# Kernel optimization log

Hardware: AMD Instinct MI355X
Metric: run time of the kernel (lower is better)

## Reference

```python
import jax, jax.numpy as jnp
import numpy as np

L, H, E, V, BS = 12, 12, 768, 50257, 1024  # layers, heads, n_embd, vocab, block_size
B, T = 2, 1024
D = E // H


def setup_inputs() -> dict:
    key = jax.random.key(0)
    ks = jax.random.split(key, 10)
    s = 0.02
    d = {}
    d["idx"] = jax.random.randint(ks[0], (B, T), 0, V)
    d["targets"] = jax.random.randint(ks[1], (B, T), 0, V)
    # embeddings (wte tied with lm_head)
    d["wte"] = (jax.random.normal(ks[2], (V, E)) * s).astype(jnp.float32)
    d["wpe"] = (jax.random.normal(ks[3], (BS, E)) * s).astype(jnp.float32)
    # stacked per-layer params; Linear weights stored [in, out] (= torch W.T)
    d["ln1_w"] = jnp.ones((L, E), jnp.float32)
    d["ln1_b"] = jnp.zeros((L, E), jnp.float32)
    d["attn_w"] = (jax.random.normal(ks[4], (L, E, 3 * E)) * s).astype(jnp.float32)
    d["attn_b"] = jnp.zeros((L, 3 * E), jnp.float32)
    d["proj_w"] = (jax.random.normal(ks[5], (L, E, E)) * s).astype(jnp.float32)
    d["proj_b"] = jnp.zeros((L, E), jnp.float32)
    d["ln2_w"] = jnp.ones((L, E), jnp.float32)
    d["ln2_b"] = jnp.zeros((L, E), jnp.float32)
    d["fc_w"] = (jax.random.normal(ks[6], (L, E, 4 * E)) * s).astype(jnp.float32)
    d["fc_b"] = jnp.zeros((L, 4 * E), jnp.float32)
    d["fcproj_w"] = (jax.random.normal(ks[7], (L, 4 * E, E)) * s).astype(jnp.float32)
    d["fcproj_b"] = jnp.zeros((L, E), jnp.float32)
    d["lnf_w"] = jnp.ones((E,), jnp.float32)
    d["lnf_b"] = jnp.zeros((E,), jnp.float32)
    return d


def _ln(x, w, b, eps=1e-5):
    m = jnp.mean(x, -1, keepdims=True)
    v = jnp.mean(jnp.square(x - m), -1, keepdims=True)
    return (x - m) * jax.lax.rsqrt(v + eps) * w + b


def _block(x, p, mask):
    l1w, l1b, aw, ab, pw, pb, l2w, l2b, fw, fb, fpw, fpb = p
    Bx, Tx, C = x.shape
    # causal self-attention (explicit QK^T + mask + softmax + AV, as in source)
    qkv = _ln(x, l1w, l1b) @ aw + ab                       # [B,T,3E]
    q, k, v = jnp.split(qkv, 3, axis=-1)
    q = q.reshape(Bx, Tx, H, D).transpose(0, 2, 1, 3)       # [B,H,T,D]
    k = k.reshape(Bx, Tx, H, D).transpose(0, 2, 1, 3)
    v = v.reshape(Bx, Tx, H, D).transpose(0, 2, 1, 3)
    att = jnp.einsum('bhqd,bhkd->bhqk', q, k) * (1.0 / np.sqrt(D))
    att = jnp.where(mask, att, -jnp.inf)
    att = jax.nn.softmax(att, axis=-1)
    y = jnp.einsum('bhqk,bhkd->bhqd', att, v)
    y = y.transpose(0, 2, 1, 3).reshape(Bx, Tx, C)
    x = x + y @ pw + pb
    # MLP with tanh-approx GELU
    h = jax.nn.gelu(_ln(x, l2w, l2b) @ fw + fb, approximate=True)
    x = x + h @ fpw + fpb
    return x


def reference(idx, targets, wte, wpe, ln1_w, ln1_b, attn_w, attn_b, proj_w, proj_b,
              ln2_w, ln2_b, fc_w, fc_b, fcproj_w, fcproj_b, lnf_w, lnf_b):
    Tq = idx.shape[1]
    x = wte[idx] + wpe[:Tq]                                 # [B,T,E]
    mask = jnp.tril(jnp.ones((Tq, Tq), dtype=bool))

    def step(x, p):
        return _block(x, p, mask), None

    layer_params = (ln1_w, ln1_b, attn_w, attn_b, proj_w, proj_b,
                    ln2_w, ln2_b, fc_w, fc_b, fcproj_w, fcproj_b)
    x, _ = jax.lax.scan(step, x, layer_params)
    x = _ln(x, lnf_w, lnf_b)
    logits = x @ wte.T                                      # tied lm_head, [B,T,V]
    logp = jax.nn.log_softmax(logits, axis=-1)
    nll = -jnp.take_along_axis(logp, targets[..., None], axis=-1)[..., 0]
    loss = jnp.mean(nll)
    return logits, loss
```

## Files before the change

### kernel.cpp

```cpp
#include <hip/hip_runtime.h>
#include <hip/hip_bf16.h>
#include <math.h>

#define LNUM 12
#define HNUM 12
#define EDIM 768
#define VDIM 50257
#define BDIM 2
#define TDIM 1024
#define BT (BDIM*TDIM)
#define E3 (3*EDIM)
#define E4 (4*EDIM)
#define NPB (2*((VDIM+127)/128))

typedef __bf16 bf16x8 __attribute__((ext_vector_type(8)));
typedef float f32x4 __attribute__((ext_vector_type(4)));

__device__ __forceinline__ float gelu_f(float x) {
    float u = 0.7978845608028654f * (x + 0.044715f * x * x * x);
    return 0.5f * x * (1.0f + tanhf(u));
}

__device__ __forceinline__ void gl16(const void* g, void* l) {
    __builtin_amdgcn_global_load_lds(
        (const __attribute__((address_space(1))) unsigned int*)g,
        (__attribute__((address_space(3))) unsigned int*)l,
        16, 0, 0);
}

__global__ __launch_bounds__(256) void embed_kernel(
    const int* __restrict__ idx, const float* __restrict__ wte,
    const float* __restrict__ wpe, float* __restrict__ x)
{
    const int row = blockIdx.x;
    const int t = row % TDIM;
    const int tok = idx[row];
    const float* we = wte + (size_t)tok * EDIM;
    const float* pe = wpe + (size_t)t * EDIM;
    float* xr = x + (size_t)row * EDIM;
    for (int e = threadIdx.x; e < EDIM; e += 256) xr[e] = we[e] + pe[e];
}

__global__ __launch_bounds__(256) void ln_kernel(
    const float* __restrict__ in, const float* __restrict__ w,
    const float* __restrict__ b, __bf16* __restrict__ out)
{
    const int row = blockIdx.x, tid = threadIdx.x;
    const float* xr = in + (size_t)row * EDIM;
    float v0 = xr[tid], v1 = xr[tid + 256], v2 = xr[tid + 512];
    float s = v0 + v1 + v2;
    __shared__ float red[8];
    const int lane = tid & 63, wid = tid >> 6;
    #pragma unroll
    for (int off = 32; off; off >>= 1) s += __shfl_xor(s, off);
    if (lane == 0) red[wid] = s;
    __syncthreads();
    const float mean = (red[0] + red[1] + red[2] + red[3]) * (1.0f / EDIM);
    float d0 = v0 - mean, d1 = v1 - mean, d2 = v2 - mean;
    float s2 = d0 * d0 + d1 * d1 + d2 * d2;
    #pragma unroll
    for (int off = 32; off; off >>= 1) s2 += __shfl_xor(s2, off);
    if (lane == 0) red[4 + wid] = s2;
    __syncthreads();
    const float var = (red[4] + red[5] + red[6] + red[7]) * (1.0f / EDIM);
    const float inv = rsqrtf(var + 1e-5f);
    __bf16* orow = out + (size_t)row * EDIM;
    orow[tid]       = (__bf16)(d0 * inv * w[tid]       + b[tid]);
    orow[tid + 256] = (__bf16)(d1 * inv * w[tid + 256] + b[tid + 256]);
    orow[tid + 512] = (__bf16)(d2 * inv * w[tid + 512] + b[tid + 512]);
}

__global__ __launch_bounds__(256) void convt_kernel(
    const float* __restrict__ in, __bf16* __restrict__ out, int K, int N)
{
    in  += (size_t)blockIdx.z * K * N;
    out += (size_t)blockIdx.z * K * N;
    __shared__ float t[32][33];
    const int n0 = blockIdx.x * 32, k0 = blockIdx.y * 32;
    const int tx = threadIdx.x & 31, ty = threadIdx.x >> 5;
    #pragma unroll
    for (int r = ty; r < 32; r += 8)
        t[r][tx] = in[(size_t)(k0 + r) * N + n0 + tx];
    __syncthreads();
    #pragma unroll
    for (int r = ty; r < 32; r += 8)
        out[(size_t)(n0 + r) * K + k0 + tx] = (__bf16)t[tx][r];
}

__global__ __launch_bounds__(256) void cvt_kernel(
    const float* __restrict__ in, __bf16* __restrict__ out, long n4)
{
    for (long i = blockIdx.x * 256L + threadIdx.x; i < n4; i += (long)gridDim.x * 256L) {
        float4 v = ((const float4*)in)[i];
        out[i * 4 + 0] = (__bf16)v.x;
        out[i * 4 + 1] = (__bf16)v.y;
        out[i * 4 + 2] = (__bf16)v.z;
        out[i * 4 + 3] = (__bf16)v.w;
    }
}

template<int BM, int BN, int BK, bool BIAS, bool GELU_, bool RES_, bool OUTBF, bool NGUARD, bool LOGITS>
__global__ __launch_bounds__(256) void mgemm(
    const __bf16* __restrict__ A, const __bf16* __restrict__ Bt,
    const float* __restrict__ bias, const float* __restrict__ res,
    void* __restrict__ Cout, float* __restrict__ part, int M, int N, int K)
{
    constexpr int WM = BM / 2, WN = BN / 2;
    constexpr int FM = WM / 16, FN = WN / 16;
    constexpr int KS = BK / 32;
    constexpr int TB = BM * BK * 2;
    constexpr int rA = TB / 4096, rB = (BN * BK * 2) / 4096;
    constexpr int RPI = 2048 / BK;
    constexpr int CPR = BK / 8;
    __shared__ __align__(16) __bf16 As[3 * BM * BK];
    __shared__ __align__(16) __bf16 Bs[3 * BN * BK];
    const int tid = threadIdx.x;
    const int lane = tid & 63;
    const int wave = tid >> 6;
    const int wr = wave >> 1, wc = wave & 1;

    int bm, bn;
    if (LOGITS) {
        const int wg = blockIdx.x;
        bn = (wg & 7) + ((wg >> 7) << 3);
        bm = (wg >> 3) & 15;
        if (bn * BN >= N) return;
    } else { bm = blockIdx.y; bn = blockIdx.x; }
    const int m0 = bm * BM;
    const int n0 = bn * BN;

    const int srow = tid / CPR;
    const int skey = (BK == 32) ? ((srow >> 1) & 3) : (srow & 7);
    const int c0 = (tid % CPR) ^ skey;

    const __bf16* gA = A + (size_t)(m0 + srow) * K + c0 * 8;
    const __bf16* gB[rB];
    #pragma unroll
    for (int r = 0; r < rB; ++r) {
        int nr = n0 + srow + r * RPI;
        if (NGUARD) nr = nr < N ? nr : N - 1;
        gB[r] = Bt + (size_t)nr * K + c0 * 8;
    }

    const int fr = lane & 15;
    const int g = lane >> 4;
    const int fkey = (BK == 32) ? ((fr >> 1) & 3) : (fr & 7);

    f32x4 acc[FM][FN];
    #pragma unroll
    for (int i = 0; i < FM; i++)
        #pragma unroll
        for (int j = 0; j < FN; j++) acc[i][j] = (f32x4){0.f, 0.f, 0.f, 0.f};

    const int nt = K / BK;

    auto stage = [&](int kk, int b) {
        #pragma unroll
        for (int r = 0; r < rA; ++r)
            gl16(gA + (size_t)r * RPI * K + kk, (char*)As + b * TB + r * 4096 + tid * 16);
        #pragma unroll
        for (int r = 0; r < rB; ++r)
            gl16(gB[r] + kk, (char*)Bs + b * TB + r * 4096 + tid * 16);
    };

    stage(0, 0);
    if (nt > 1) stage(BK, 1);

    int b0 = 0, b1 = 1, b2 = 2;
    for (int t = 0; t < nt; ++t) {
        if (t + 1 < nt) {
            static_assert(rA + rB == 4, "vmcnt literal assumes 4 loads/stage");
            asm volatile("s_waitcnt vmcnt(4)" ::: "memory");
        } else {
            asm volatile("s_waitcnt vmcnt(0)" ::: "memory");
        }
        asm volatile("s_barrier" ::: "memory");
        if (t + 2 < nt) stage((t + 2) * BK, b2);

        const char* pa = (const char*)As + b0 * TB;
        const char* pb = (const char*)Bs + b0 * TB;
        bf16x8 af[FM][KS], bfr[FN][KS];
        #pragma unroll
        for (int i = 0; i < FM; i++)
            #pragma unroll
            for (int kc = 0; kc < KS; kc++)
                af[i][kc] = *(const bf16x8*)(pa + (wr * WM + i * 16 + fr) * (2 * BK)
                                                + (((kc * 4 + g) ^ fkey) << 4));
        #pragma unroll
        for (int j = 0; j < FN; j++)
            #pragma unroll
            for (int kc = 0; kc < KS; kc++)
                bfr[j][kc] = *(const bf16x8*)(pb + (wc * WN + j * 16 + fr) * (2 * BK)
                                                 + (((kc * 4 + g) ^ fkey) << 4));
        #pragma unroll
        for (int kc = 0; kc < KS; kc++)
            #pragma unroll
            for (int i = 0; i < FM; i++)
                #pragma unroll
                for (int j = 0; j < FN; j++)
                    acc[i][j] = __builtin_amdgcn_mfma_f32_16x16x32_bf16(af[i][kc], bfr[j][kc], acc[i][j], 0, 0, 0);
        const int tmp = b0; b0 = b1; b1 = b2; b2 = tmp;
    }

    const int crow = g * 4;
    if (LOGITS) {
        const int bn2 = bn * 2 + wc;
        #pragma unroll
        for (int i = 0; i < FM; i++) {
            #pragma unroll
            for (int r = 0; r < 4; r++) {
                const int m = m0 + wr * WM + i * 16 + crow + r;
                float se = 0.f;
                #pragma unroll
                for (int j = 0; j < FN; j++) {
                    const int n = n0 + wc * WN + j * 16 + fr;
                    if (n < N) {
                        float v = acc[i][j][r];
                        ((float*)Cout)[(size_t)m * N + n] = v;
                        se += __expf(v);
                    }
                }
                se += __shfl_xor(se, 1); se += __shfl_xor(se, 2);
                se += __shfl_xor(se, 4); se += __shfl_xor(se, 8);
                if (fr == 0) part[(size_t)m * NPB + bn2] = se;
            }
        }
    } else {
        #pragma unroll
        for (int i = 0; i < FM; i++) {
            #pragma unroll
            for (int r = 0; r < 4; r++) {
                const int m = m0 + wr * WM + i * 16 + crow + r;
                #pragma unroll
                for (int j = 0; j < FN; j++) {
                    const int n = n0 + wc * WN + j * 16 + fr;
                    if (!NGUARD || n < N) {
                        float v = acc[i][j][r];
                        if (BIAS) v += bias[n];
                        if (GELU_) v = gelu_f(v);
                        if (RES_) v += res[(size_t)m * N + n];
                        if (OUTBF) ((__bf16*)Cout)[(size_t)m * N + n] = (__bf16)v;
                        else       ((float*)Cout)[(size_t)m * N + n] = v;
                    }
                }
            }
        }
    }
}

__global__ __launch_bounds__(256) void fattn_kernel(
    const __bf16* __restrict__ qkv, __bf16* __restrict__ y)
{
    const int bq = blockIdx.x, h = blockIdx.y, b = blockIdx.z;
    const int tid = threadIdx.x, lane = tid & 63, w = tid >> 6;
    const int fr = lane & 15, g = lane >> 4;

    __shared__ __align__(16) __bf16 Ks[64 * 64];
    __shared__ __align__(16) __bf16 Vt[64 * 64];
    __shared__ __align__(16) __bf16 Ps[4][16 * 64];

    const __bf16* base = qkv + (size_t)b * TDIM * E3;
    const int q0w = bq * 64 + w * 16;

    bf16x8 qf[2];
    {
        const __bf16* qp = base + (size_t)(q0w + fr) * E3 + h * 64 + g * 8;
        qf[0] = *(const bf16x8*)qp;
        qf[1] = *(const bf16x8*)(qp + 32);
    }

    const int r0 = tid >> 3, ch = tid & 7;
    bf16x8 kr[2], vr[2];

    #pragma unroll
    for (int it = 0; it < 2; ++it) {
        const int row = it * 32 + r0;
        const __bf16* gp = base + (size_t)row * E3 + EDIM + h * 64 + ch * 8;
        kr[it] = *(const bf16x8*)gp;
        vr[it] = *(const bf16x8*)(gp + EDIM);
    }
    #pragma unroll
    for (int it = 0; it < 2; ++it) {
        const int row = it * 32 + r0;
        *(bf16x8*)(Ks + row * 64 + ((ch ^ (row & 7)) << 3)) = kr[it];
        #pragma unroll
        for (int j = 0; j < 8; ++j) {
            const int d = ch * 8 + j;
            const int key = ((d >> 3) ^ d) & 7;
            Vt[d * 64 + ((((row >> 3) ^ key) << 3) + (row & 7))] = vr[it][j];
        }
    }
    __syncthreads();

    float m[4] = {-1e30f, -1e30f, -1e30f, -1e30f};
    float l[4] = {0.f, 0.f, 0.f, 0.f};
    f32x4 acc[4];
    #pragma unroll
    for (int jd = 0; jd < 4; ++jd) acc[jd] = (f32x4){0.f, 0.f, 0.f, 0.f};

    for (int kt = 0; kt <= bq; ++kt) {
        if (kt < bq) {
            const int k1 = (kt + 1) * 64;
            #pragma unroll
            for (int it = 0; it < 2; ++it) {
                const int row = it * 32 + r0;
                const __bf16* gp = base + (size_t)(k1 + row) * E3 + EDIM + h * 64 + ch * 8;
                kr[it] = *(const bf16x8*)gp;
                vr[it] = *(const bf16x8*)(gp + EDIM);
            }
        }

        const int k0 = kt * 64;
        f32x4 s[4];
        #pragma unroll
        for (int jf = 0; jf < 4; ++jf) {
            const int krow = jf * 16 + fr;
            f32x4 sv = (f32x4){0.f, 0.f, 0.f, 0.f};
            #pragma unroll
            for (int kc = 0; kc < 2; ++kc) {
                bf16x8 kf = *(const bf16x8*)(Ks + krow * 64 + (((kc * 4 + g) ^ (fr & 7)) << 3));
                sv = __builtin_amdgcn_mfma_f32_16x16x32_bf16(qf[kc], kf, sv, 0, 0, 0);
            }
            s[jf] = sv;
        }
        #pragma unroll
        for (int jf = 0; jf < 4; ++jf)
            #pragma unroll
            for (int r = 0; r < 4; ++r) s[jf][r] *= 0.125f;
        if (kt == bq) {
            #pragma unroll
            for (int jf = 0; jf < 4; ++jf) {
                const int k = k0 + jf * 16 + fr;
                #pragma unroll
                for (int r = 0; r < 4; ++r) {
                    const int q = q0w + g * 4 + r;
                    if (k > q) s[jf][r] = -1e30f;
                }
            }
        }

        #pragma unroll
        for (int r = 0; r < 4; ++r) {
            float mx = fmaxf(fmaxf(s[0][r], s[1][r]), fmaxf(s[2][r], s[3][r]));
            mx = fmaxf(mx, __shfl_xor(mx, 1));
            mx = fmaxf(mx, __shfl_xor(mx, 2));
            mx = fmaxf(mx, __shfl_xor(mx, 4));
            mx = fmaxf(mx, __shfl_xor(mx, 8));
            const float mn = fmaxf(m[r], mx);
            const float sc2 = __expf(m[r] - mn);
            m[r] = mn;
            float rs = 0.f;
            #pragma unroll
            for (int jf = 0; jf < 4; ++jf) {
                const float p = __expf(s[jf][r] - mn);
                s[jf][r] = p;
                rs += p;
            }
            rs += __shfl_xor(rs, 1);
            rs += __shfl_xor(rs, 2);
            rs += __shfl_xor(rs, 4);
            rs += __shfl_xor(rs, 8);
            l[r] = l[r] * sc2 + rs;
            #pragma unroll
            for (int jd = 0; jd < 4; ++jd) acc[jd][r] *= sc2;
        }

        __bf16* pw = &Ps[w][0];
        #pragma unroll
        for (int jf = 0; jf < 4; ++jf) {
            const int chp = jf * 2 + (fr >> 3);
            #pragma unroll
            for (int r = 0; r < 4; ++r) {
                const int row = g * 4 + r;
                pw[row * 64 + (((chp ^ (row & 7)) << 3) + (fr & 7))] = (__bf16)s[jf][r];
            }
        }
        asm volatile("s_waitcnt lgkmcnt(0)" ::: "memory");
        bf16x8 pa[2];
        #pragma unroll
        for (int kc = 0; kc < 2; ++kc)
            pa[kc] = *(const bf16x8*)(pw + fr * 64 + (((kc * 4 + g) ^ (fr & 7)) << 3));

        #pragma unroll
        for (int jd = 0; jd < 4; ++jd) {
            const int d = jd * 16 + fr;
            const int key = ((d >> 3) ^ d) & 7;
            #pragma unroll
            for (int kc = 0; kc < 2; ++kc) {
                bf16x8 vf = *(const bf16x8*)(Vt + d * 64 + (((kc * 4 + g) ^ key) << 3));
                acc[jd] = __builtin_amdgcn_mfma_f32_16x16x32_bf16(pa[kc], vf, acc[jd], 0, 0, 0);
            }
        }

        if (kt < bq) {
            __syncthreads();
            #pragma unroll
            for (int it = 0; it < 2; ++it) {
                const int row = it * 32 + r0;
                *(bf16x8*)(Ks + row * 64 + ((ch ^ (row & 7)) << 3)) = kr[it];
                #pragma unroll
                for (int j = 0; j < 8; ++j) {
                    const int d = ch * 8 + j;
                    const int key = ((d >> 3) ^ d) & 7;
                    Vt[d * 64 + ((((row >> 3) ^ key) << 3) + (row & 7))] = vr[it][j];
                }
            }
            __syncthreads();
        }
    }

    #pragma unroll
    for (int r = 0; r < 4; ++r) {
        const float inv = 1.0f / l[r];
        const int q = q0w + g * 4 + r;
        __bf16* yp = y + ((size_t)(b * TDIM + q)) * EDIM + h * 64;
        #pragma unroll
        for (int jd = 0; jd < 4; ++jd)
            yp[jd * 16 + fr] = (__bf16)(acc[jd][r] * inv);
    }
}

__global__ __launch_bounds__(256) void lsefin_kernel(
    const float* __restrict__ part, const float* __restrict__ logits,
    const int* __restrict__ targets, float* __restrict__ rr)
{
    const int row = blockIdx.x, tid = threadIdx.x;
    float s = 0.f;
    for (int j = tid; j < NPB; j += 256) s += part[(size_t)row * NPB + j];
    #pragma unroll
    for (int off = 32; off; off >>= 1) s += __shfl_xor(s, off);
    __shared__ float red[4];
    if ((tid & 63) == 0) red[tid >> 6] = s;
    __syncthreads();
    if (tid == 0) {
        float S = red[0] + red[1] + red[2] + red[3];
        rr[row] = logf(S) - logits[(size_t)row * VDIM + targets[row]];
    }
}

__global__ __launch_bounds__(256) void loss_reduce_kernel(
    const float* __restrict__ rr, float* __restrict__ out)
{
    const int tid = threadIdx.x;
    float s = 0.f;
    for (int i = tid; i < BT; i += 256) s += rr[i];
    #pragma unroll
    for (int off = 32; off; off >>= 1) s += __shfl_xor(s, off);
    __shared__ float red[4];
    if ((tid & 63) == 0) red[tid >> 6] = s;
    __syncthreads();
    if (tid == 0) out[0] = (red[0] + red[1] + red[2] + red[3]) * (1.0f / BT);
}

extern "C" void kernel_launch(void* const* d_in, const int* in_sizes, int n_in,
                              void* d_out, int out_size, void* d_ws, size_t ws_size,
                              hipStream_t stream)
{
    const int*   idx     = (const int*)d_in[0];
    const int*   targets = (const int*)d_in[1];
    const float* wte     = (const float*)d_in[2];
    const float* wpe     = (const float*)d_in[3];
    const float* ln1_w   = (const float*)d_in[4];
    const float* ln1_b   = (const float*)d_in[5];
    const float* attn_w  = (const float*)d_in[6];
    const float* attn_b  = (const float*)d_in[7];
    const float* proj_w  = (const float*)d_in[8];
    const float* proj_b  = (const float*)d_in[9];
    const float* ln2_w   = (const float*)d_in[10];
    const float* ln2_b   = (const float*)d_in[11];
    const float* fc_w    = (const float*)d_in[12];
    const float* fc_b    = (const float*)d_in[13];
    const float* fcp_w   = (const float*)d_in[14];
    const float* fcp_b   = (const float*)d_in[15];
    const float* lnf_w   = (const float*)d_in[16];
    const float* lnf_b   = (const float*)d_in[17];

    float* logits = (float*)d_out;

    const size_t slq = (size_t)EDIM * E3, slp = (size_t)EDIM * EDIM;
    const size_t slf = (size_t)EDIM * E4, slfp = (size_t)E4 * EDIM;

    char* wp = (char*)d_ws;
    float*  x     = (float*)wp;   wp += (size_t)BT * EDIM * 4;
    __bf16* qkvb  = (__bf16*)wp;  wp += (size_t)BT * E3 * 2;
    __bf16* xnbf  = (__bf16*)wp;  wp += (size_t)BT * EDIM * 2;
    __bf16* ybf   = (__bf16*)wp;  wp += (size_t)BT * EDIM * 2;
    __bf16* hbf   = (__bf16*)wp;  wp += (size_t)BT * E4 * 2;
    __bf16* wteb  = (__bf16*)wp;  wp += (size_t)VDIM * EDIM * 2;
    float*  part  = (float*)wp;   wp += (size_t)BT * NPB * 4;
    float*  rr    = (float*)wp;   wp += (size_t)BT * 4;
    __bf16* wqkvb = (__bf16*)wp;

    const size_t wbytes_all = (slq + slp + slf + slfp) * 2 * LNUM;
    const size_t used = (size_t)(wp - (char*)d_ws);
    const bool big = ws_size >= used + wbytes_all;
    const size_t L = big ? LNUM : 1;
    __bf16* wprjb = wqkvb + slq * L;
    __bf16* wfcb  = wprjb + slp * L;
    __bf16* wfpb  = wfcb  + slf * L;

    embed_kernel<<<BT, 256, 0, stream>>>(idx, wte, wpe, x);
    cvt_kernel<<<2048, 256, 0, stream>>>(wte, wteb, (long)VDIM * EDIM / 4);

    if (big) {
        convt_kernel<<<dim3(E3 / 32, EDIM / 32, LNUM), 256, 0, stream>>>(attn_w, wqkvb, EDIM, E3);
        convt_kernel<<<dim3(EDIM / 32, EDIM / 32, LNUM), 256, 0, stream>>>(proj_w, wprjb, EDIM, EDIM);
        convt_kernel<<<dim3(E4 / 32, EDIM / 32, LNUM), 256, 0, stream>>>(fc_w, wfcb, EDIM, E4);
        convt_kernel<<<dim3(EDIM / 32, E4 / 32, LNUM), 256, 0, stream>>>(fcp_w, wfpb, E4, EDIM);
    }

    for (int l = 0; l < LNUM; ++l) {
        const __bf16* wq = wqkvb + (big ? (size_t)l * slq : 0);
        const __bf16* wpj = wprjb + (big ? (size_t)l * slp : 0);
        const __bf16* wf = wfcb + (big ? (size_t)l * slf : 0);
        const __bf16* wfp = wfpb + (big ? (size_t)l * slfp : 0);

        ln_kernel<<<BT, 256, 0, stream>>>(x, ln1_w + (size_t)l * EDIM,
                                          ln1_b + (size_t)l * EDIM, xnbf);
        if (!big)
            convt_kernel<<<dim3(E3 / 32, EDIM / 32), 256, 0, stream>>>(
                attn_w + (size_t)l * slq, (__bf16*)wq, EDIM, E3);
        mgemm<128, 128, 32, true, false, false, true, false, false>
            <<<dim3(E3 / 128, BT / 128), 256, 0, stream>>>(
            xnbf, wq, attn_b + (size_t)l * E3, nullptr, qkvb, nullptr, BT, E3, EDIM);
        fattn_kernel<<<dim3(TDIM / 64, HNUM, BDIM), 256, 0, stream>>>(qkvb, ybf);
        if (!big)
            convt_kernel<<<dim3(EDIM / 32, EDIM / 32), 256, 0, stream>>>(
                proj_w + (size_t)l * slp, (__bf16*)wpj, EDIM, EDIM);
        mgemm<64, 64, 64, true, false, true, false, false, false>
            <<<dim3(EDIM / 64, BT / 64), 256, 0, stream>>>(
            ybf, wpj, proj_b + (size_t)l * EDIM, x, x, nullptr, BT, EDIM, EDIM);
        ln_kernel<<<BT, 256, 0, stream>>>(x, ln2_w + (size_t)l * EDIM,
                                          ln2_b + (size_t)l * EDIM, xnbf);
        if (!big)
            convt_kernel<<<dim3(E4 / 32, EDIM / 32), 256, 0, stream>>>(
                fc_w + (size_t)l * slf, (__bf16*)wf, EDIM, E4);
        mgemm<128, 128, 32, true, true, false, true, false, false>
            <<<dim3(E4 / 128, BT / 128), 256, 0, stream>>>(
            xnbf, wf, fc_b + (size_t)l * E4, nullptr, hbf, nullptr, BT, E4, EDIM);
        if (!big)
            convt_kernel<<<dim3(EDIM / 32, E4 / 32), 256, 0, stream>>>(
                fcp_w + (size_t)l * slfp, (__bf16*)wfp, E4, EDIM);
        mgemm<64, 64, 64, true, false, true, false, false, false>
            <<<dim3(EDIM / 64, BT / 64), 256, 0, stream>>>(
            hbf, wfp, fcp_b + (size_t)l * EDIM, x, x, nullptr, BT, EDIM, E4);
    }

    ln_kernel<<<BT, 256, 0, stream>>>(x, lnf_w, lnf_b, xnbf);
    mgemm<128, 128, 32, false, false, false, false, true, true>
        <<<dim3(16 * 400), 256, 0, stream>>>(
        xnbf, wteb, nullptr, nullptr, logits, part, BT, VDIM, EDIM);
    lsefin_kernel<<<BT, 256, 0, stream>>>(part, logits, targets, rr);
    loss_reduce_kernel<<<1, 256, 0, stream>>>(rr, logits + (size_t)BT * VDIM);
}
```

Baseline: 2.264 ms.

## Use 256x128 tiles for logits GEMM and a one-wave-per-row LayerNorm

```diff
diff --git a/kernel.cpp b/kernel.cpp
--- a/kernel.cpp
+++ b/kernel.cpp
@@ -14,6 +14,7 @@
 #define NPB (2*((VDIM+127)/128))
 
 typedef __bf16 bf16x8 __attribute__((ext_vector_type(8)));
+typedef __bf16 bf16x4 __attribute__((ext_vector_type(4)));
 typedef float f32x4 __attribute__((ext_vector_type(4)));
 
 __device__ __forceinline__ float gelu_f(float x) {
@@ -45,29 +46,38 @@
     const float* __restrict__ in, const float* __restrict__ w,
     const float* __restrict__ b, __bf16* __restrict__ out)
 {
-    const int row = blockIdx.x, tid = threadIdx.x;
-    const float* xr = in + (size_t)row * EDIM;
-    float v0 = xr[tid], v1 = xr[tid + 256], v2 = xr[tid + 512];
-    float s = v0 + v1 + v2;
-    __shared__ float red[8];
-    const int lane = tid & 63, wid = tid >> 6;
+    const int row = blockIdx.x * 4 + (threadIdx.x >> 6);
+    const int lane = threadIdx.x & 63;
+    const float4* xr = (const float4*)(in + (size_t)row * EDIM);
+    float4 a0 = xr[lane], a1 = xr[64 + lane], a2 = xr[128 + lane];
+    float s = a0.x + a0.y + a0.z + a0.w + a1.x + a1.y + a1.z + a1.w
+            + a2.x + a2.y + a2.z + a2.w;
     #pragma unroll
     for (int off = 32; off; off >>= 1) s += __shfl_xor(s, off);
-    if (lane == 0) red[wid] = s;
-    __syncthreads();
-    const float mean = (red[0] + red[1] + red[2] + red[3]) * (1.0f / EDIM);
-    float d0 = v0 - mean, d1 = v1 - mean, d2 = v2 - mean;
-    float s2 = d0 * d0 + d1 * d1 + d2 * d2;
-    #pragma unroll
-    for (int off = 32; off; off >>= 1) s2 += __shfl_xor(s2, off);
-    if (lane == 0) red[4 + wid] = s2;
-    __syncthreads();
-    const float var = (red[4] + red[5] + red[6] + red[7]) * (1.0f / EDIM);
-    const float inv = rsqrtf(var + 1e-5f);
+    const float mean = s * (1.0f / EDIM);
+    float4 d0 = make_float4(a0.x - mean, a0.y - mean, a0.z - mean, a0.w - mean);
+    float4 d1 = make_float4(a1.x - mean, a1.y - mean, a1.z - mean, a1.w - mean);
+    float4 d2 = make_float4(a2.x - mean, a2.y - mean, a2.z - mean, a2.w - mean);
+    float v = d0.x*d0.x + d0.y*d0.y + d0.z*d0.z + d0.w*d0.w
+            + d1.x*d1.x + d1.y*d1.y + d1.z*d1.z + d1.w*d1.w
+            + d2.x*d2.x + d2.y*d2.y + d2.z*d2.z + d2.w*d2.w;
+    #pragma unroll
+    for (int off = 32; off; off >>= 1) v += __shfl_xor(v, off);
+    const float inv = rsqrtf(v * (1.0f / EDIM) + 1e-5f);
+    const float4* w4 = (const float4*)w;
+    const float4* b4 = (const float4*)b;
     __bf16* orow = out + (size_t)row * EDIM;
-    orow[tid]       = (__bf16)(d0 * inv * w[tid]       + b[tid]);
-    orow[tid + 256] = (__bf16)(d1 * inv * w[tid + 256] + b[tid + 256]);
-    orow[tid + 512] = (__bf16)(d2 * inv * w[tid + 512] + b[tid + 512]);
+    #pragma unroll
+    for (int c = 0; c < 3; ++c) {
+        float4 dd = c == 0 ? d0 : (c == 1 ? d1 : d2);
+        float4 ww = w4[c * 64 + lane], bb = b4[c * 64 + lane];
+        bf16x4 o;
+        o[0] = (__bf16)(dd.x * inv * ww.x + bb.x);
+        o[1] = (__bf16)(dd.y * inv * ww.y + bb.y);
+        o[2] = (__bf16)(dd.z * inv * ww.z + bb.z);
+        o[3] = (__bf16)(dd.w * inv * ww.w + bb.w);
+        *(bf16x4*)(orow + c * 256 + lane * 4) = o;
+    }
 }
 
 __global__ __launch_bounds__(256) void convt_kernel(
@@ -100,7 +110,7 @@
 }
 
 template<int BM, int BN, int BK, bool BIAS, bool GELU_, bool RES_, bool OUTBF, bool NGUARD, bool LOGITS>
-__global__ __launch_bounds__(256) void mgemm(
+__global__ __launch_bounds__(256, 2) void mgemm(
     const __bf16* __restrict__ A, const __bf16* __restrict__ Bt,
     const float* __restrict__ bias, const float* __restrict__ res,
     void* __restrict__ Cout, float* __restrict__ part, int M, int N, int K)
@@ -108,8 +118,9 @@
     constexpr int WM = BM / 2, WN = BN / 2;
     constexpr int FM = WM / 16, FN = WN / 16;
     constexpr int KS = BK / 32;
-    constexpr int TB = BM * BK * 2;
-    constexpr int rA = TB / 4096, rB = (BN * BK * 2) / 4096;
+    constexpr int TBA = BM * BK * 2;
+    constexpr int TBB = BN * BK * 2;
+    constexpr int rA = TBA / 4096, rB = TBB / 4096;
     constexpr int RPI = 2048 / BK;
     constexpr int CPR = BK / 8;
     __shared__ __align__(16) __bf16 As[3 * BM * BK];
@@ -122,8 +133,8 @@
     int bm, bn;
     if (LOGITS) {
         const int wg = blockIdx.x;
-        bn = (wg & 7) + ((wg >> 7) << 3);
-        bm = (wg >> 3) & 15;
+        bm = (wg >> 3) & 7;
+        bn = (wg & 7) + ((wg >> 6) << 3);
         if (bn * BN >= N) return;
     } else { bm = blockIdx.y; bn = blockIdx.x; }
     const int m0 = bm * BM;
@@ -157,10 +168,10 @@
     auto stage = [&](int kk, int b) {
         #pragma unroll
         for (int r = 0; r < rA; ++r)
-            gl16(gA + (size_t)r * RPI * K + kk, (char*)As + b * TB + r * 4096 + tid * 16);
+            gl16(gA + (size_t)r * RPI * K + kk, (char*)As + b * TBA + r * 4096 + tid * 16);
         #pragma unroll
         for (int r = 0; r < rB; ++r)
-            gl16(gB[r] + kk, (char*)Bs + b * TB + r * 4096 + tid * 16);
+            gl16(gB[r] + kk, (char*)Bs + b * TBB + r * 4096 + tid * 16);
     };
 
     stage(0, 0);
@@ -169,16 +180,17 @@
     int b0 = 0, b1 = 1, b2 = 2;
     for (int t = 0; t < nt; ++t) {
         if (t + 1 < nt) {
-            static_assert(rA + rB == 4, "vmcnt literal assumes 4 loads/stage");
-            asm volatile("s_waitcnt vmcnt(4)" ::: "memory");
+            static_assert(rA + rB == 4 || rA + rB == 6, "vmcnt literal");
+            if constexpr (rA + rB == 4) asm volatile("s_waitcnt vmcnt(4)" ::: "memory");
+            else                        asm volatile("s_waitcnt vmcnt(6)" ::: "memory");
         } else {
             asm volatile("s_waitcnt vmcnt(0)" ::: "memory");
         }
         asm volatile("s_barrier" ::: "memory");
         if (t + 2 < nt) stage((t + 2) * BK, b2);
 
-        const char* pa = (const char*)As + b0 * TB;
-        const char* pb = (const char*)Bs + b0 * TB;
+        const char* pa = (const char*)As + b0 * TBA;
+        const char* pb = (const char*)Bs + b0 * TBB;
         bf16x8 af[FM][KS], bfr[FN][KS];
         #pragma unroll
         for (int i = 0; i < FM; i++)
@@ -515,8 +527,8 @@
         const __bf16* wf = wfcb + (big ? (size_t)l * slf : 0);
         const __bf16* wfp = wfpb + (big ? (size_t)l * slfp : 0);
 
-        ln_kernel<<<BT, 256, 0, stream>>>(x, ln1_w + (size_t)l * EDIM,
-                                          ln1_b + (size_t)l * EDIM, xnbf);
+        ln_kernel<<<BT / 4, 256, 0, stream>>>(x, ln1_w + (size_t)l * EDIM,
+                                              ln1_b + (size_t)l * EDIM, xnbf);
         if (!big)
             convt_kernel<<<dim3(E3 / 32, EDIM / 32), 256, 0, stream>>>(
                 attn_w + (size_t)l * slq, (__bf16*)wq, EDIM, E3);
@@ -530,8 +542,8 @@
         mgemm<64, 64, 64, true, false, true, false, false, false>
             <<<dim3(EDIM / 64, BT / 64), 256, 0, stream>>>(
             ybf, wpj, proj_b + (size_t)l * EDIM, x, x, nullptr, BT, EDIM, EDIM);
-        ln_kernel<<<BT, 256, 0, stream>>>(x, ln2_w + (size_t)l * EDIM,
-                                          ln2_b + (size_t)l * EDIM, xnbf);
+        ln_kernel<<<BT / 4, 256, 0, stream>>>(x, ln2_w + (size_t)l * EDIM,
+                                              ln2_b + (size_t)l * EDIM, xnbf);
         if (!big)
             convt_kernel<<<dim3(E4 / 32, EDIM / 32), 256, 0, stream>>>(
                 fc_w + (size_t)l * slf, (__bf16*)wf, EDIM, E4);
@@ -546,9 +558,9 @@
             hbf, wfp, fcp_b + (size_t)l * EDIM, x, x, nullptr, BT, EDIM, E4);
     }
 
-    ln_kernel<<<BT, 256, 0, stream>>>(x, lnf_w, lnf_b, xnbf);
-    mgemm<128, 128, 32, false, false, false, false, true, true>
-        <<<dim3(16 * 400), 256, 0, stream>>>(
+    ln_kernel<<<BT / 4, 256, 0, stream>>>(x, lnf_w, lnf_b, xnbf);
+    mgemm<256, 128, 32, false, false, false, false, true, true>
+        <<<dim3(64 * 50), 256, 0, stream>>>(
         xnbf, wteb, nullptr, nullptr, logits, part, BT, VDIM, EDIM);
     lsefin_kernel<<<BT, 256, 0, stream>>>(part, logits, targets, rr);
     loss_reduce_kernel<<<1, 256, 0, stream>>>(rr, logits + (size_t)BT * VDIM);
```

After: 2.256 ms. About the same (-0.4%).
